# Performance work log

Measured on AMD Instinct MI355X. Metric: run time of the kernel, lower is better.

## Reference

```python
import jax, jax.numpy as jnp
import numpy as np

B, S, E, H = 4, 1024, 1024, 16
HD = E // H


def setup_inputs() -> dict:
    key = jax.random.key(0)
    k1, k2, k3 = jax.random.split(key, 3)
    hidden_states = jax.random.normal(k1, (B, S, E), dtype=jnp.float32)
    attention_mask = jnp.ones((B, S), dtype=jnp.int32)
    STD = 0.02
    W_qkv = jax.random.normal(k2, (E, 3 * E), dtype=jnp.float32) * STD
    b_qkv = jnp.zeros((3 * E,), dtype=jnp.float32)
    W_proj = jax.random.normal(k3, (E, E), dtype=jnp.float32) * STD
    b_proj = jnp.zeros((E,), dtype=jnp.float32)
    return {
        "hidden_states": hidden_states,
        "attention_mask": attention_mask,
        "W_qkv": W_qkv,
        "b_qkv": b_qkv,
        "W_proj": W_proj,
        "b_proj": b_proj,
    }


def reference(hidden_states, attention_mask, W_qkv, b_qkv, W_proj, b_proj):
    b, s, _ = hidden_states.shape
    dtype = hidden_states.dtype
    qkv = hidden_states @ W_qkv + b_qkv  # [b, s, 3E]
    q, k, v = jnp.split(qkv, 3, axis=-1)

    def split_heads(x):
        return x.reshape(b, s, H, HD).transpose(0, 2, 1, 3)  # [b, H, s, hd]

    q, k, v = split_heads(q), split_heads(k), split_heads(v)
    scale = jnp.asarray(HD, dtype=dtype) ** (-0.5)
    scores = jnp.einsum("bnth,bnsh->bnts", q, k) * scale  # [b, H, s, s]
    causal = jnp.tril(jnp.ones((s, s), dtype=bool))
    key_mask = attention_mask.astype(bool)  # [b, s]
    full_mask = causal[None, None, :, :] & key_mask[:, None, None, :]
    neg = jnp.asarray(jnp.finfo(dtype).min, dtype=dtype)
    bias = jnp.where(full_mask, jnp.asarray(0.0, dtype=dtype), neg)
    probs = jax.nn.softmax(scores + bias, axis=-1)
    out = jnp.einsum("bnts,bnsh->bnth", probs, v)  # [b, H, s, hd]
    out = out.transpose(0, 2, 1, 3).reshape(b, s, E)
    return out @ W_proj + b_proj
```

## Files before the change

### kernel.cpp

```cpp
#include <hip/hip_runtime.h>
#include <stdint.h>

typedef __attribute__((ext_vector_type(8))) short bf16x8;
typedef __attribute__((ext_vector_type(4))) float f32x4;
typedef unsigned short u16;

__device__ __forceinline__ float bf2f(u16 b) {
    unsigned int u = ((unsigned int)b) << 16;
    return __builtin_bit_cast(float, u);
}
__device__ __forceinline__ u16 f2bf(float f) {
    unsigned int u = __builtin_bit_cast(unsigned int, f);
    u += 0x7fffu + ((u >> 16) & 1u);
    return (u16)(u >> 16);
}
__device__ __forceinline__ u16 f2bf_trunc(float f) {
    return (u16)(__builtin_bit_cast(unsigned int, f) >> 16);
}

__device__ __forceinline__ void gl2lds16(const u16* g, u16* l) {
    __builtin_amdgcn_global_load_lds(
        (const __attribute__((address_space(1))) unsigned int*)g,
        (__attribute__((address_space(3))) unsigned int*)l, 16, 0, 0);
}

__global__ __launch_bounds__(256) void prep_kernel(
    const float* __restrict__ hs, const float* __restrict__ Wqkv,
    const float* __restrict__ Wproj, u16* __restrict__ hs_bf,
    u16* __restrict__ wqkv_t, u16* __restrict__ wproj_t) {
    __shared__ float t[64][68];
    int bx = blockIdx.x, tid = threadIdx.x;
    if (bx < 4096) {
        long i = ((long)bx * 256 + tid) * 4;
        float4 v = *(const float4*)(hs + i);
        alignas(8) u16 o[4] = {f2bf(v.x), f2bf(v.y), f2bf(v.z), f2bf(v.w)};
        *(uint2*)(hs_bf + i) = *(const uint2*)o;
        return;
    }
    const float* in;
    u16* out;
    int R = 1024, C, c0, r0;
    if (bx < 4864) {
        int tt = bx - 4096;
        C = 3072; c0 = (tt % 48) * 64; r0 = (tt / 48) * 64;
        in = Wqkv; out = wqkv_t;
    } else {
        int tt = bx - 4864;
        C = 1024; c0 = (tt % 16) * 64; r0 = (tt / 16) * 64;
        in = Wproj; out = wproj_t;
    }
#pragma unroll
    for (int i = 0; i < 4; i++) {
        int ch = i * 256 + tid;
        int r = ch >> 4, cc = (ch & 15) * 4;
        float4 v = *(const float4*)(in + (long)(r0 + r) * C + c0 + cc);
        *(float4*)&t[r][cc] = v;
    }
    __syncthreads();
#pragma unroll
    for (int i = 0; i < 2; i++) {
        int ch = i * 256 + tid;
        int cw = ch >> 3, rr = (ch & 7) * 8;
        alignas(16) u16 tmp[8];
#pragma unroll
        for (int j = 0; j < 8; j++) tmp[j] = f2bf(t[rr + j][cw]);
        *(int4*)(out + (long)(c0 + cw) * R + r0 + rr) = *(const int4*)tmp;
    }
}

__global__ __launch_bounds__(256) void gemm_qkv(
    const u16* __restrict__ X, const u16* __restrict__ Wt,
    const float* __restrict__ bias, const int* __restrict__ amask,
    u16* __restrict__ q_ws, u16* __restrict__ k_ws, u16* __restrict__ vt_ws,
    int K) {
    __shared__ u16 As[128 * 32];
    __shared__ u16 Bs[128 * 32];
    const int tid = threadIdx.x;
    const int m0 = blockIdx.y * 128, n0 = blockIdx.x * 128;
    const int w = tid >> 6, lane = tid & 63, l16 = lane & 15, quad = lane >> 4;
    const int wm = (w >> 1) * 64, wn = (w & 1) * 64;

    f32x4 acc[4][4];
    const f32x4 z = {0.f, 0.f, 0.f, 0.f};
#pragma unroll
    for (int i = 0; i < 4; i++)
#pragma unroll
        for (int j = 0; j < 4; j++) acc[i][j] = z;

    for (int k0 = 0; k0 < K; k0 += 32) {
        if (k0) __syncthreads();
#pragma unroll
        for (int i = 0; i < 2; i++) {
            int slot = i * 256 + tid;
            int row = slot >> 2, gp = slot & 3;
            int g = gp ^ ((row >> 1) & 3);
            gl2lds16(X + (long)(m0 + row) * K + k0 + g * 8, &As[slot * 8]);
            gl2lds16(Wt + (long)(n0 + row) * K + k0 + g * 8, &Bs[slot * 8]);
        }
        __syncthreads();
        bf16x8 af[4], bfr[4];
#pragma unroll
        for (int mt = 0; mt < 4; mt++) {
            int row = wm + mt * 16 + l16;
            int g = quad ^ ((row >> 1) & 3);
            af[mt] = *(const bf16x8*)&As[row * 32 + g * 8];
        }
#pragma unroll
        for (int nt = 0; nt < 4; nt++) {
            int row = wn + nt * 16 + l16;
            int g = quad ^ ((row >> 1) & 3);
            bfr[nt] = *(const bf16x8*)&Bs[row * 32 + g * 8];
        }
#pragma unroll
        for (int mt = 0; mt < 4; mt++)
#pragma unroll
            for (int nt = 0; nt < 4; nt++)
                acc[mt][nt] = __builtin_amdgcn_mfma_f32_16x16x32_bf16(
                    af[mt], bfr[nt], acc[mt][nt], 0, 0, 0);
    }

    const int which = n0 >> 10;
    const int b = m0 >> 10;
    int ncol[4]; float bv[4];
#pragma unroll
    for (int nt = 0; nt < 4; nt++) {
        ncol[nt] = n0 + wn + nt * 16 + l16;
        bv[nt] = bias[ncol[nt]];
    }
#pragma unroll
    for (int mt = 0; mt < 4; mt++) {
#pragma unroll
        for (int r = 0; r < 4; r++) {
            int m = m0 + wm + mt * 16 + quad * 4 + r;
            int s = m & 1023;
            float mk = 1.f;
            if (which == 2) mk = amask[b * 1024 + s] ? 1.f : 0.f;
#pragma unroll
            for (int nt = 0; nt < 4; nt++) {
                int e = ncol[nt] & 1023, h = e >> 6, d = e & 63;
                float val = acc[mt][nt][r] + bv[nt];
                if (which == 0)
                    q_ws[((long)(b * 16 + h) * 1024 + s) * 64 + d] = f2bf(val);
                else if (which == 1)
                    k_ws[((long)(b * 16 + h) * 1024 + s) * 64 + d] = f2bf(val);
                else
                    vt_ws[((long)(b * 16 + h) * 65 + d) * 1024 + s] = f2bf(val * mk);
            }
        }
    }
    if (which == 2) {
        int hh = ((n0 & 1023) >> 6) + (tid >> 7);
        int s = (m0 & 1023) + (tid & 127);
        vt_ws[((long)(b * 16 + hh) * 65 + 64) * 1024 + s] =
            amask[b * 1024 + s] ? (u16)0x3F80 : (u16)0;
    }
}

#define PPAD 88
__global__ __launch_bounds__(256) void attn_kernel(
    const u16* __restrict__ Q, const u16* __restrict__ K,
    const u16* __restrict__ Vt, u16* __restrict__ O) {
    const int S = 1024;
    const int idx = blockIdx.x;
    const int qb = 15 - (idx >> 6);
    const int bh = idx & 63, b = bh >> 4, h = bh & 15;
    const int tid = threadIdx.x, w = tid >> 6, lane = tid & 63;
    const int l16 = lane & 15, quad = lane >> 4;
    const int q0 = qb * 64 + w * 16;

    __shared__ u16 kt[2][64 * 64];
    __shared__ u16 vt[2][80 * 64];
    __shared__ u16 p_lds[4][16][PPAD];

    const u16* Qb = Q + (long)bh * S * 64;
    const u16* Kb = K + (long)bh * S * 64;
    const u16* Vb = Vt + (long)bh * 65 * S;

    if (tid < 240) {
        int bufi = tid >= 120, rem = tid - bufi * 120;
        int row = 65 + (rem >> 3), gp = rem & 7;
        const int4 z4 = {0, 0, 0, 0};
        *(int4*)&vt[bufi][row * 64 + gp * 8] = z4;
    }

    const float C = 0.125f * 1.4426950408889634f;
    bf16x8 qf[2];
#pragma unroll
    for (int kc = 0; kc < 2; kc++) {
        bf16x8 qr = *(const bf16x8*)(Qb + (q0 + l16) * 64 + kc * 32 + quad * 8);
        bf16x8 qs;
#pragma unroll
        for (int e = 0; e < 8; e++) qs[e] = (short)f2bf(bf2f((u16)qr[e]) * C);
        qf[kc] = qs;
    }

    const f32x4 z = {0.f, 0.f, 0.f, 0.f};
    f32x4 o_acc[5];
#pragma unroll
    for (int nt = 0; nt < 5; nt++) o_acc[nt] = z;

    auto prefetch = [&](int j, int pb) {
        int4 mrow;
        if (tid < 8)
            mrow = *(const int4*)(Vb + 64 * S + j * 64 + tid * 8);
#pragma unroll
        for (int i = 0; i < 2; i++) {
            int slot = i * 256 + tid;
            int row = slot >> 3, gp = slot & 7;
            int g = gp ^ (row & 7);
            gl2lds16(Kb + (j * 64 + row) * 64 + g * 8, &kt[pb][slot * 8]);
        }
#pragma unroll
        for (int i = 0; i < 2; i++) {
            int slot = i * 256 + tid;
            int row = slot >> 3, gp = slot & 7;
            int g = gp ^ (row & 7);
            gl2lds16(Vb + (long)row * S + j * 64 + g * 8, &vt[pb][slot * 8]);
        }
        if (tid < 8)
            *(int4*)&vt[pb][64 * 64 + tid * 8] = mrow;
    };

    prefetch(0, 0);
    for (int j = 0; j <= qb; j++) {
        int buf = j & 1;
        __syncthreads();
        if (j < qb) prefetch(j + 1, buf ^ 1);

        f32x4 s_acc[4];
#pragma unroll
        for (int nt = 0; nt < 4; nt++) s_acc[nt] = z;
#pragma unroll
        for (int nt = 0; nt < 4; nt++) {
            int row = nt * 16 + l16;
#pragma unroll
            for (int kc = 0; kc < 2; kc++) {
                int g = (kc * 4 + quad) ^ (row & 7);
                bf16x8 kf = *(const bf16x8*)&kt[buf][row * 64 + g * 8];
                s_acc[nt] = __builtin_amdgcn_mfma_f32_16x16x32_bf16(qf[kc], kf, s_acc[nt], 0, 0, 0);
            }
        }
        float p[4][4];
#pragma unroll
        for (int nt = 0; nt < 4; nt++)
#pragma unroll
            for (int r = 0; r < 4; r++) p[nt][r] = exp2f(s_acc[nt][r]);
        if (j == qb) {
#pragma unroll
            for (int nt = 0; nt < 4; nt++) {
                int key = j * 64 + nt * 16 + l16;
#pragma unroll
                for (int r = 0; r < 4; r++)
                    if (key > q0 + quad * 4 + r) p[nt][r] = 0.f;
            }
        }
#pragma unroll
        for (int nt = 0; nt < 4; nt++)
#pragma unroll
            for (int r = 0; r < 4; r++)
                p_lds[w][quad * 4 + r][nt * 16 + l16] = f2bf_trunc(p[nt][r]);
        bf16x8 pf[2];
#pragma unroll
        for (int kc = 0; kc < 2; kc++)
            pf[kc] = *(const bf16x8*)&p_lds[w][l16][kc * 32 + quad * 8];
#pragma unroll
        for (int nt = 0; nt < 5; nt++) {
            int row = nt * 16 + l16;
#pragma unroll
            for (int kc = 0; kc < 2; kc++) {
                int g = (kc * 4 + quad) ^ (row & 7);
                bf16x8 vf = *(const bf16x8*)&vt[buf][row * 64 + g * 8];
                o_acc[nt] = __builtin_amdgcn_mfma_f32_16x16x32_bf16(pf[kc], vf, o_acc[nt], 0, 0, 0);
            }
        }
    }
#pragma unroll
    for (int r = 0; r < 4; r++) {
        float l = __shfl(o_acc[4][r], lane & 48, 64);
        float inv = 1.0f / l;
        int qg = q0 + quad * 4 + r;
#pragma unroll
        for (int nt = 0; nt < 4; nt++)
            O[((long)(b * S + qg)) * 1024 + h * 64 + nt * 16 + l16] = f2bf(o_acc[nt][r] * inv);
    }
}

__global__ __launch_bounds__(256) void gemm_proj(
    const u16* __restrict__ X, const u16* __restrict__ Wt,
    const float* __restrict__ bias, float* __restrict__ outF, int K) {
    __shared__ u16 As[128 * 32];
    __shared__ u16 Bs[64 * 32];
    const int tid = threadIdx.x;
    const int m0 = blockIdx.y * 128, n0 = blockIdx.x * 64;
    const int w = tid >> 6, lane = tid & 63, l16 = lane & 15, quad = lane >> 4;
    const int wm = (w >> 1) * 64, wn = (w & 1) * 32;
    const int N = 1024;

    f32x4 acc[4][2];
    const f32x4 z = {0.f, 0.f, 0.f, 0.f};
#pragma unroll
    for (int i = 0; i < 4; i++)
#pragma unroll
        for (int j = 0; j < 2; j++) acc[i][j] = z;

    for (int k0 = 0; k0 < K; k0 += 32) {
        if (k0) __syncthreads();
#pragma unroll
        for (int i = 0; i < 2; i++) {
            int slot = i * 256 + tid;
            int row = slot >> 2, gp = slot & 3;
            int g = gp ^ ((row >> 1) & 3);
            gl2lds16(X + (long)(m0 + row) * K + k0 + g * 8, &As[slot * 8]);
        }
        {
            int slot = tid;
            int row = slot >> 2, gp = slot & 3;
            int g = gp ^ ((row >> 1) & 3);
            gl2lds16(Wt + (long)(n0 + row) * K + k0 + g * 8, &Bs[slot * 8]);
        }
        __syncthreads();
        bf16x8 af[4], bfr[2];
#pragma unroll
        for (int mt = 0; mt < 4; mt++) {
            int row = wm + mt * 16 + l16;
            int g = quad ^ ((row >> 1) & 3);
            af[mt] = *(const bf16x8*)&As[row * 32 + g * 8];
        }
#pragma unroll
        for (int nt = 0; nt < 2; nt++) {
            int row = wn + nt * 16 + l16;
            int g = quad ^ ((row >> 1) & 3);
            bfr[nt] = *(const bf16x8*)&Bs[row * 32 + g * 8];
        }
#pragma unroll
        for (int mt = 0; mt < 4; mt++)
#pragma unroll
            for (int nt = 0; nt < 2; nt++)
                acc[mt][nt] = __builtin_amdgcn_mfma_f32_16x16x32_bf16(
                    af[mt], bfr[nt], acc[mt][nt], 0, 0, 0);
    }
#pragma unroll
    for (int nt = 0; nt < 2; nt++) {
        int n = n0 + wn + nt * 16 + l16;
        float bias_v = bias[n];
#pragma unroll
        for (int mt = 0; mt < 4; mt++)
#pragma unroll
            for (int r = 0; r < 4; r++) {
                int m = m0 + wm + mt * 16 + quad * 4 + r;
                outF[(long)m * N + n] = acc[mt][nt][r] + bias_v;
            }
    }
}

extern "C" void kernel_launch(void* const* d_in, const int* in_sizes, int n_in,
                              void* d_out, int out_size, void* d_ws, size_t ws_size,
                              hipStream_t stream) {
    const float* hs    = (const float*)d_in[0];
    const int*   amask = (const int*)d_in[1];
    const float* Wqkv  = (const float*)d_in[2];
    const float* bqkv  = (const float*)d_in[3];
    const float* Wproj = (const float*)d_in[4];
    const float* bproj = (const float*)d_in[5];
    float* out = (float*)d_out;

    const long ME = 4096L * 1024L;
    const long VT = 65L * 1024L * 64L;
    size_t need = (3072L * 1024 + ME + 1024L * 1024 + 2 * ME + VT) * 2;
    if (ws_size < need) return;

    u16* wqkv_t  = (u16*)d_ws;
    u16* hs_bf   = wqkv_t + 3072L * 1024;
    u16* wproj_t = hs_bf + ME;
    u16* q_ws    = wproj_t + 1024L * 1024;
    u16* k_ws    = q_ws + ME;
    u16* vt_ws   = k_ws + ME;
    u16* attn_out= (u16*)d_ws;

    dim3 blk(256);
    prep_kernel<<<dim3(5120), blk, 0, stream>>>(hs, Wqkv, Wproj, hs_bf, wqkv_t, wproj_t);
    gemm_qkv<<<dim3(24, 32), blk, 0, stream>>>(hs_bf, wqkv_t, bqkv, amask,
                                               q_ws, k_ws, vt_ws, 1024);
    attn_kernel<<<dim3(1024), blk, 0, stream>>>(q_ws, k_ws, vt_ws, attn_out);
    gemm_proj<<<dim3(16, 32), blk, 0, stream>>>(attn_out, wproj_t, bproj, out, 1024);
}
```

Baseline: 174.9 us.

## Load GEMM MFMA fragments directly from global memory with register double buffering

Both the QKV and output-projection GEMMs stop staging tiles in LDS and drop their __syncthreads barriers. Each lane now loads its bf16x8 MFMA fragments straight from global memory and prefetches the next k-slice into a second register set while the current slice's MFMAs run. K is also hard-coded to 1024 so the loop fully unrolls. The cost is that tiles are no longer shared across waves: the two waves that use the same A or B rows each fetch them from global/L2, and each lane reads a 16-byte strided chunk rather than a coalesced row, which may be worse for memory traffic than the LDS version.

After: 261.4 us. 49.4% more time.

```diff
diff --git a/kernel.cpp b/kernel.cpp
--- a/kernel.cpp
+++ b/kernel.cpp
@@ -71,15 +71,22 @@
 __global__ __launch_bounds__(256) void gemm_qkv(
     const u16* __restrict__ X, const u16* __restrict__ Wt,
     const float* __restrict__ bias, const int* __restrict__ amask,
-    u16* __restrict__ q_ws, u16* __restrict__ k_ws, u16* __restrict__ vt_ws,
-    int K) {
-    __shared__ u16 As[128 * 32];
-    __shared__ u16 Bs[128 * 32];
+    u16* __restrict__ q_ws, u16* __restrict__ k_ws, u16* __restrict__ vt_ws) {
+    const int K = 1024;
     const int tid = threadIdx.x;
     const int m0 = blockIdx.y * 128, n0 = blockIdx.x * 128;
     const int w = tid >> 6, lane = tid & 63, l16 = lane & 15, quad = lane >> 4;
     const int wm = (w >> 1) * 64, wn = (w & 1) * 64;
 
+    const u16* pa[4];
+    const u16* pb[4];
+#pragma unroll
+    for (int mt = 0; mt < 4; mt++)
+        pa[mt] = X + (long)(m0 + wm + mt * 16 + l16) * K + quad * 8;
+#pragma unroll
+    for (int nt = 0; nt < 4; nt++)
+        pb[nt] = Wt + (long)(n0 + wn + nt * 16 + l16) * K + quad * 8;
+
     f32x4 acc[4][4];
     const f32x4 z = {0.f, 0.f, 0.f, 0.f};
 #pragma unroll
@@ -87,36 +94,40 @@
 #pragma unroll
         for (int j = 0; j < 4; j++) acc[i][j] = z;
 
-    for (int k0 = 0; k0 < K; k0 += 32) {
-        if (k0) __syncthreads();
-#pragma unroll
-        for (int i = 0; i < 2; i++) {
-            int slot = i * 256 + tid;
-            int row = slot >> 2, gp = slot & 3;
-            int g = gp ^ ((row >> 1) & 3);
-            gl2lds16(X + (long)(m0 + row) * K + k0 + g * 8, &As[slot * 8]);
-            gl2lds16(Wt + (long)(n0 + row) * K + k0 + g * 8, &Bs[slot * 8]);
-        }
-        __syncthreads();
-        bf16x8 af[4], bfr[4];
-#pragma unroll
-        for (int mt = 0; mt < 4; mt++) {
-            int row = wm + mt * 16 + l16;
-            int g = quad ^ ((row >> 1) & 3);
-            af[mt] = *(const bf16x8*)&As[row * 32 + g * 8];
-        }
-#pragma unroll
-        for (int nt = 0; nt < 4; nt++) {
-            int row = wn + nt * 16 + l16;
-            int g = quad ^ ((row >> 1) & 3);
-            bfr[nt] = *(const bf16x8*)&Bs[row * 32 + g * 8];
+    bf16x8 a0[4], b0[4], a1[4], b1[4];
+#pragma unroll
+    for (int t = 0; t < 4; t++) {
+        a0[t] = *(const bf16x8*)(pa[t]);
+        b0[t] = *(const bf16x8*)(pb[t]);
+    }
+#pragma unroll
+    for (int k0 = 0; k0 < K; k0 += 64) {
+        if (k0 + 32 < K) {
+#pragma unroll
+            for (int t = 0; t < 4; t++) {
+                a1[t] = *(const bf16x8*)(pa[t] + k0 + 32);
+                b1[t] = *(const bf16x8*)(pb[t] + k0 + 32);
+            }
         }
 #pragma unroll
         for (int mt = 0; mt < 4; mt++)
 #pragma unroll
             for (int nt = 0; nt < 4; nt++)
                 acc[mt][nt] = __builtin_amdgcn_mfma_f32_16x16x32_bf16(
-                    af[mt], bfr[nt], acc[mt][nt], 0, 0, 0);
+                    a0[mt], b0[nt], acc[mt][nt], 0, 0, 0);
+        if (k0 + 64 < K) {
+#pragma unroll
+            for (int t = 0; t < 4; t++) {
+                a0[t] = *(const bf16x8*)(pa[t] + k0 + 64);
+                b0[t] = *(const bf16x8*)(pb[t] + k0 + 64);
+            }
+        }
+#pragma unroll
+        for (int mt = 0; mt < 4; mt++)
+#pragma unroll
+            for (int nt = 0; nt < 4; nt++)
+                acc[mt][nt] = __builtin_amdgcn_mfma_f32_16x16x32_bf16(
+                    a1[mt], b1[nt], acc[mt][nt], 0, 0, 0);
     }
 
     const int which = n0 >> 10;
@@ -287,14 +298,21 @@
 
 __global__ __launch_bounds__(256) void gemm_proj(
     const u16* __restrict__ X, const u16* __restrict__ Wt,
-    const float* __restrict__ bias, float* __restrict__ outF, int K) {
-    __shared__ u16 As[128 * 32];
-    __shared__ u16 Bs[64 * 32];
+    const float* __restrict__ bias, float* __restrict__ outF) {
+    const int K = 1024, N = 1024;
     const int tid = threadIdx.x;
     const int m0 = blockIdx.y * 128, n0 = blockIdx.x * 64;
     const int w = tid >> 6, lane = tid & 63, l16 = lane & 15, quad = lane >> 4;
     const int wm = (w >> 1) * 64, wn = (w & 1) * 32;
-    const int N = 1024;
+
+    const u16* pa[4];
+    const u16* pb[2];
+#pragma unroll
+    for (int mt = 0; mt < 4; mt++)
+        pa[mt] = X + (long)(m0 + wm + mt * 16 + l16) * K + quad * 8;
+#pragma unroll
+    for (int nt = 0; nt < 2; nt++)
+        pb[nt] = Wt + (long)(n0 + wn + nt * 16 + l16) * K + quad * 8;
 
     f32x4 acc[4][2];
     const f32x4 z = {0.f, 0.f, 0.f, 0.f};
@@ -303,41 +321,37 @@
 #pragma unroll
         for (int j = 0; j < 2; j++) acc[i][j] = z;
 
-    for (int k0 = 0; k0 < K; k0 += 32) {
-        if (k0) __syncthreads();
-#pragma unroll
-        for (int i = 0; i < 2; i++) {
-            int slot = i * 256 + tid;
-            int row = slot >> 2, gp = slot & 3;
-            int g = gp ^ ((row >> 1) & 3);
-            gl2lds16(X + (long)(m0 + row) * K + k0 + g * 8, &As[slot * 8]);
-        }
-        {
-            int slot = tid;
-            int row = slot >> 2, gp = slot & 3;
-            int g = gp ^ ((row >> 1) & 3);
-            gl2lds16(Wt + (long)(n0 + row) * K + k0 + g * 8, &Bs[slot * 8]);
-        }
-        __syncthreads();
-        bf16x8 af[4], bfr[2];
-#pragma unroll
-        for (int mt = 0; mt < 4; mt++) {
-            int row = wm + mt * 16 + l16;
-            int g = quad ^ ((row >> 1) & 3);
-            af[mt] = *(const bf16x8*)&As[row * 32 + g * 8];
-        }
-#pragma unroll
-        for (int nt = 0; nt < 2; nt++) {
-            int row = wn + nt * 16 + l16;
-            int g = quad ^ ((row >> 1) & 3);
-            bfr[nt] = *(const bf16x8*)&Bs[row * 32 + g * 8];
+    bf16x8 a0[4], b0[2], a1[4], b1[2];
+#pragma unroll
+    for (int t = 0; t < 4; t++) a0[t] = *(const bf16x8*)(pa[t]);
+#pragma unroll
+    for (int t = 0; t < 2; t++) b0[t] = *(const bf16x8*)(pb[t]);
+#pragma unroll
+    for (int k0 = 0; k0 < K; k0 += 64) {
+        if (k0 + 32 < K) {
+#pragma unroll
+            for (int t = 0; t < 4; t++) a1[t] = *(const bf16x8*)(pa[t] + k0 + 32);
+#pragma unroll
+            for (int t = 0; t < 2; t++) b1[t] = *(const bf16x8*)(pb[t] + k0 + 32);
         }
 #pragma unroll
         for (int mt = 0; mt < 4; mt++)
 #pragma unroll
             for (int nt = 0; nt < 2; nt++)
                 acc[mt][nt] = __builtin_amdgcn_mfma_f32_16x16x32_bf16(
-                    af[mt], bfr[nt], acc[mt][nt], 0, 0, 0);
+                    a0[mt], b0[nt], acc[mt][nt], 0, 0, 0);
+        if (k0 + 64 < K) {
+#pragma unroll
+            for (int t = 0; t < 4; t++) a0[t] = *(const bf16x8*)(pa[t] + k0 + 64);
+#pragma unroll
+            for (int t = 0; t < 2; t++) b0[t] = *(const bf16x8*)(pb[t] + k0 + 64);
+        }
+#pragma unroll
+        for (int mt = 0; mt < 4; mt++)
+#pragma unroll
+            for (int nt = 0; nt < 2; nt++)
+                acc[mt][nt] = __builtin_amdgcn_mfma_f32_16x16x32_bf16(
+                    a1[mt], b1[nt], acc[mt][nt], 0, 0, 0);
     }
 #pragma unroll
     for (int nt = 0; nt < 2; nt++) {
@@ -379,8 +393,7 @@
 
     dim3 blk(256);
     prep_kernel<<<dim3(5120), blk, 0, stream>>>(hs, Wqkv, Wproj, hs_bf, wqkv_t, wproj_t);
-    gemm_qkv<<<dim3(24, 32), blk, 0, stream>>>(hs_bf, wqkv_t, bqkv, amask,
-                                               q_ws, k_ws, vt_ws, 1024);
+    gemm_qkv<<<dim3(24, 32), blk, 0, stream>>>(hs_bf, wqkv_t, bqkv, amask, q_ws, k_ws, vt_ws);
     attn_kernel<<<dim3(1024), blk, 0, stream>>>(q_ws, k_ws, vt_ws, attn_out);
-    gemm_proj<<<dim3(16, 32), blk, 0, stream>>>(attn_out, wproj_t, bproj, out, 1024);
-}
+    gemm_proj<<<dim3(16, 32), blk, 0, stream>>>(attn_out, wproj_t, bproj, out);
+}
```

## Double-buffer LDS tiles in QKV and projection GEMMs to overlap loads

Applied to the files above, without the earlier changes.

Both GEMM kernels now keep two shared-memory tile buffers and prefetch the next K-slice via global_load_lds while MFMAs consume the current one. This halves the barriers per iteration and aims to hide global memory latency behind compute. K is hardcoded to 1024, and LDS usage doubles, which may reduce occupancy.

Result: slower. 181.9 us (+4.0%).

```diff
diff --git a/kernel.cpp b/kernel.cpp
--- a/kernel.cpp
+++ b/kernel.cpp
@@ -71,10 +71,10 @@
 __global__ __launch_bounds__(256) void gemm_qkv(
     const u16* __restrict__ X, const u16* __restrict__ Wt,
     const float* __restrict__ bias, const int* __restrict__ amask,
-    u16* __restrict__ q_ws, u16* __restrict__ k_ws, u16* __restrict__ vt_ws,
-    int K) {
-    __shared__ u16 As[128 * 32];
-    __shared__ u16 Bs[128 * 32];
+    u16* __restrict__ q_ws, u16* __restrict__ k_ws, u16* __restrict__ vt_ws) {
+    const int K = 1024;
+    __shared__ u16 As[2][128 * 32];
+    __shared__ u16 Bs[2][128 * 32];
     const int tid = threadIdx.x;
     const int m0 = blockIdx.y * 128, n0 = blockIdx.x * 128;
     const int w = tid >> 6, lane = tid & 63, l16 = lane & 15, quad = lane >> 4;
@@ -87,29 +87,34 @@
 #pragma unroll
         for (int j = 0; j < 4; j++) acc[i][j] = z;
 
-    for (int k0 = 0; k0 < K; k0 += 32) {
-        if (k0) __syncthreads();
+    auto stage = [&](int k0, int pb) {
 #pragma unroll
         for (int i = 0; i < 2; i++) {
             int slot = i * 256 + tid;
             int row = slot >> 2, gp = slot & 3;
             int g = gp ^ ((row >> 1) & 3);
-            gl2lds16(X + (long)(m0 + row) * K + k0 + g * 8, &As[slot * 8]);
-            gl2lds16(Wt + (long)(n0 + row) * K + k0 + g * 8, &Bs[slot * 8]);
-        }
+            gl2lds16(X + (long)(m0 + row) * K + k0 + g * 8, &As[pb][slot * 8]);
+            gl2lds16(Wt + (long)(n0 + row) * K + k0 + g * 8, &Bs[pb][slot * 8]);
+        }
+    };
+
+    stage(0, 0);
+    for (int it = 0; it < 32; it++) {
+        int buf = it & 1;
         __syncthreads();
+        if (it + 1 < 32) stage((it + 1) * 32, buf ^ 1);
         bf16x8 af[4], bfr[4];
 #pragma unroll
         for (int mt = 0; mt < 4; mt++) {
             int row = wm + mt * 16 + l16;
             int g = quad ^ ((row >> 1) & 3);
-            af[mt] = *(const bf16x8*)&As[row * 32 + g * 8];
+            af[mt] = *(const bf16x8*)&As[buf][row * 32 + g * 8];
         }
 #pragma unroll
         for (int nt = 0; nt < 4; nt++) {
             int row = wn + nt * 16 + l16;
             int g = quad ^ ((row >> 1) & 3);
-            bfr[nt] = *(const bf16x8*)&Bs[row * 32 + g * 8];
+            bfr[nt] = *(const bf16x8*)&Bs[buf][row * 32 + g * 8];
         }
 #pragma unroll
         for (int mt = 0; mt < 4; mt++)
@@ -287,14 +292,14 @@
 
 __global__ __launch_bounds__(256) void gemm_proj(
     const u16* __restrict__ X, const u16* __restrict__ Wt,
-    const float* __restrict__ bias, float* __restrict__ outF, int K) {
-    __shared__ u16 As[128 * 32];
-    __shared__ u16 Bs[64 * 32];
+    const float* __restrict__ bias, float* __restrict__ outF) {
+    const int K = 1024, N = 1024;
+    __shared__ u16 As[2][128 * 32];
+    __shared__ u16 Bs[2][64 * 32];
     const int tid = threadIdx.x;
     const int m0 = blockIdx.y * 128, n0 = blockIdx.x * 64;
     const int w = tid >> 6, lane = tid & 63, l16 = lane & 15, quad = lane >> 4;
     const int wm = (w >> 1) * 64, wn = (w & 1) * 32;
-    const int N = 1024;
 
     f32x4 acc[4][2];
     const f32x4 z = {0.f, 0.f, 0.f, 0.f};
@@ -303,34 +308,39 @@
 #pragma unroll
         for (int j = 0; j < 2; j++) acc[i][j] = z;
 
-    for (int k0 = 0; k0 < K; k0 += 32) {
-        if (k0) __syncthreads();
+    auto stage = [&](int k0, int pb) {
 #pragma unroll
         for (int i = 0; i < 2; i++) {
             int slot = i * 256 + tid;
             int row = slot >> 2, gp = slot & 3;
             int g = gp ^ ((row >> 1) & 3);
-            gl2lds16(X + (long)(m0 + row) * K + k0 + g * 8, &As[slot * 8]);
+            gl2lds16(X + (long)(m0 + row) * K + k0 + g * 8, &As[pb][slot * 8]);
         }
         {
             int slot = tid;
             int row = slot >> 2, gp = slot & 3;
             int g = gp ^ ((row >> 1) & 3);
-            gl2lds16(Wt + (long)(n0 + row) * K + k0 + g * 8, &Bs[slot * 8]);
-        }
+            gl2lds16(Wt + (long)(n0 + row) * K + k0 + g * 8, &Bs[pb][slot * 8]);
+        }
+    };
+
+    stage(0, 0);
+    for (int it = 0; it < 32; it++) {
+        int buf = it & 1;
         __syncthreads();
+        if (it + 1 < 32) stage((it + 1) * 32, buf ^ 1);
         bf16x8 af[4], bfr[2];
 #pragma unroll
         for (int mt = 0; mt < 4; mt++) {
             int row = wm + mt * 16 + l16;
             int g = quad ^ ((row >> 1) & 3);
-            af[mt] = *(const bf16x8*)&As[row * 32 + g * 8];
+            af[mt] = *(const bf16x8*)&As[buf][row * 32 + g * 8];
         }
 #pragma unroll
         for (int nt = 0; nt < 2; nt++) {
             int row = wn + nt * 16 + l16;
             int g = quad ^ ((row >> 1) & 3);
-            bfr[nt] = *(const bf16x8*)&Bs[row * 32 + g * 8];
+            bfr[nt] = *(const bf16x8*)&Bs[buf][row * 32 + g * 8];
         }
 #pragma unroll
         for (int mt = 0; mt < 4; mt++)
@@ -379,8 +389,7 @@
 
     dim3 blk(256);
     prep_kernel<<<dim3(5120), blk, 0, stream>>>(hs, Wqkv, Wproj, hs_bf, wqkv_t, wproj_t);
-    gemm_qkv<<<dim3(24, 32), blk, 0, stream>>>(hs_bf, wqkv_t, bqkv, amask,
-                                               q_ws, k_ws, vt_ws, 1024);
+    gemm_qkv<<<dim3(24, 32), blk, 0, stream>>>(hs_bf, wqkv_t, bqkv, amask, q_ws, k_ws, vt_ws);
     attn_kernel<<<dim3(1024), blk, 0, stream>>>(q_ws, k_ws, vt_ws, attn_out);
-    gemm_proj<<<dim3(16, 32), blk, 0, stream>>>(attn_out, wproj_t, bproj, out, 1024);
-}
+    gemm_proj<<<dim3(16, 32), blk, 0, stream>>>(attn_out, wproj_t, bproj, out);
+}
```
